# Kernel tuning notes

Hardware: AMD Instinct MI355X
Metric: run time of the kernel (lower is better)

Reference implementation:

```python
import jax, jax.numpy as jnp
import numpy as np

G, NPG = 256, 128          # graphs per batch, nodes per graph
N = G * NPG                # 32768 total nodes
E = 524288                 # total directed edges; first half 'in', second half 'out'
DIN, D = 128, 256          # input feature dim, hidden dim
R = 200                    # num relations
C = 2                      # num classes
EPS = 1e-5                 # batchnorm eps


def setup_inputs() -> dict:
    key = jax.random.key(0)
    ks = jax.random.split(key, 20)

    def w(k, shape):
        fan_in = shape[-2] if len(shape) >= 2 else shape[-1]
        return jax.random.normal(k, shape, jnp.float32) / np.float32(np.sqrt(fan_in))

    return {
        "x": jax.random.normal(ks[0], (N, DIN), jnp.float32),
        "rel_emb": w(ks[1], (R, DIN)),
        # conv1: DIN -> D
        "w_in1": w(ks[2], (DIN, D)), "w_out1": w(ks[3], (DIN, D)),
        "w_loop1": w(ks[4], (DIN, D)), "w_rel1": w(ks[5], (DIN, D)),
        "loop_rel1": w(ks[6], (1, DIN)),
        "bias1": jnp.zeros((D,), jnp.float32),
        "gamma1": jnp.ones((D,), jnp.float32), "beta1": jnp.zeros((D,), jnp.float32),
        # conv2..conv5 stacked: D -> D
        "W_in": w(ks[7], (4, D, D)), "W_out": w(ks[8], (4, D, D)),
        "W_loop": w(ks[9], (4, D, D)), "W_rel": w(ks[10], (4, D, D)),
        "Loop_rel": w(ks[11], (4, 1, D)),
        "Bias": jnp.zeros((4, D), jnp.float32),
        "Gamma": jnp.ones((4, D), jnp.float32), "Beta": jnp.zeros((4, D), jnp.float32),
        # head: concat2 => Linear(4*D, C)
        "lin_w": w(ks[12], (4 * D, C)), "lin_b": jnp.zeros((C,), jnp.float32),
        # graph data (int constants)
        "edge_index": jax.random.randint(ks[13], (2, E), 0, N),
        "edge_type": jax.random.randint(ks[14], (E,), 0, R),
        "batch": jnp.repeat(jnp.arange(G, dtype=jnp.int32), NPG),
        "rel_labels": jax.random.randint(ks[15], (G,), 0, R),
    }


def _compgcn_conv(x, rel, edge_index, edge_type,
                  w_in, w_out, w_loop, w_rel, loop_rel, bias, gamma, beta):
    """One CompGCNConv layer (opn='mult', dropout=identity/eval, BN with batch stats)."""
    n = x.shape[0]
    half = edge_index.shape[1] // 2

    def direction(idx, etype, W):
        src, dst = idx[0], idx[1]
        # symmetric normalization: deg^{-1/2}[src] * deg^{-1/2}[dst]
        deg = jax.ops.segment_sum(jnp.ones_like(src, jnp.float32), src, num_segments=n)
        dinv = jnp.where(deg > 0, deg ** -0.5, 0.0)
        norm = dinv[src] * dinv[dst]                       # [half]
        msg = ((x[src] * rel[etype]) @ W) * norm[:, None]  # [half, D]
        return jax.ops.segment_sum(msg, dst, num_segments=n)

    in_res = direction(edge_index[:, :half], edge_type[:half], w_in)
    out_res = direction(edge_index[:, half:], edge_type[half:], w_out)
    loop_res = (x * loop_rel) @ w_loop                     # self-loop, loop relation, no norm

    out = (in_res + out_res + loop_res) / 3.0 + bias
    mean = out.mean(axis=0)
    var = out.var(axis=0)
    out = (out - mean) / jnp.sqrt(var + EPS) * gamma + beta
    return jax.nn.relu(out), rel @ w_rel


def reference(x, rel_emb, w_in1, w_out1, w_loop1, w_rel1, loop_rel1, bias1, gamma1, beta1,
              W_in, W_out, W_loop, W_rel, Loop_rel, Bias, Gamma, Beta,
              lin_w, lin_b, edge_index, edge_type, batch, rel_labels):
    x, r = _compgcn_conv(x, rel_emb, edge_index, edge_type,
                         w_in1, w_out1, w_loop1, w_rel1, loop_rel1, bias1, gamma1, beta1)
    for l in range(4):  # conv2..conv5 (fixed small layer loop)
        x, r = _compgcn_conv(x, r, edge_index, edge_type,
                             W_in[l], W_out[l], W_loop[l], W_rel[l],
                             Loop_rel[l], Bias[l], Gamma[l], Beta[l])

    # per-graph head/tail nodes (first two nodes of each graph) via segment offsets
    counts = jax.ops.segment_sum(jnp.ones((x.shape[0],), jnp.float32), batch, num_segments=G)
    offsets = (jnp.cumsum(counts) - counts).astype(jnp.int32)
    h_batch = x[offsets]
    t_batch = x[offsets + 1]

    pooled = jax.ops.segment_sum(x, batch, num_segments=G) / counts[:, None]
    rel_embs = r[rel_labels]

    feats = jnp.concatenate([pooled, rel_embs, h_batch, t_batch], axis=1)  # concat2 path
    return feats @ lin_w + lin_b


if __name__ == "__main__":
    out = reference(**setup_inputs())
    print(out.shape, out.dtype)
```

## Files before the change

### kernel.cpp

```cpp
#include <hip/hip_runtime.h>

#define NN 32768
#define GG 256
#define NPGN 128
#define ET 524288
#define EH 262144
#define D1 128
#define D2 256
#define RR 200

typedef unsigned short u16;
typedef __attribute__((ext_vector_type(8))) short bf16x8;
typedef __attribute__((ext_vector_type(4))) float f32x4;
typedef __attribute__((ext_vector_type(8))) unsigned short u16x8;

__device__ __forceinline__ float bf2f(u16 u) {
    union { unsigned int i; float f; } v; v.i = ((unsigned int)u) << 16; return v.f;
}
__device__ __forceinline__ u16 f2bf(float f) {
    union { unsigned int i; float f; } v; v.f = f;
    unsigned int x = v.i;
    return (u16)((x + 0x7fffu + ((x >> 16) & 1u)) >> 16);
}

__global__ void k_hist(const int* __restrict__ ei, int* __restrict__ hs_in,
                       int* __restrict__ hs_out, int* __restrict__ hd_in,
                       int* __restrict__ hd_out) {
    int e = blockIdx.x * blockDim.x + threadIdx.x;
    if (e >= ET) return;
    int s = ei[e], d = ei[ET + e];
    if (e < EH) { atomicAdd(&hs_in[s], 1);  atomicAdd(&hd_in[d], 1); }
    else        { atomicAdd(&hs_out[s], 1); atomicAdd(&hd_out[d], 1); }
}

__global__ void k_dinv(const int* __restrict__ hs_in, const int* __restrict__ hs_out,
                       float* __restrict__ dinv_in, float* __restrict__ dinv_out) {
    int n = blockIdx.x * blockDim.x + threadIdx.x;
    if (n >= NN) return;
    int a = hs_in[n], b = hs_out[n];
    dinv_in[n]  = a > 0 ? rsqrtf((float)a) : 0.f;
    dinv_out[n] = b > 0 ? rsqrtf((float)b) : 0.f;
}

__global__ __launch_bounds__(1024) void k_scan(const int* __restrict__ hist,
                                               int* __restrict__ off) {
    __shared__ int lds[1024];
    int t = threadIdx.x;
    int base = t * 32;
    int loc[32];
    int s = 0;
#pragma unroll
    for (int i = 0; i < 32; ++i) { loc[i] = s; s += hist[base + i]; }
    lds[t] = s;
    int tot = s;
    __syncthreads();
    for (int st = 1; st < 1024; st <<= 1) {
        int v = (t >= st) ? lds[t - st] : 0;
        __syncthreads();
        lds[t] += v;
        __syncthreads();
    }
    int excl = lds[t] - tot;
#pragma unroll
    for (int i = 0; i < 32; ++i) off[base + i] = excl + loc[i];
    if (t == 1023) off[NN] = lds[1023];
}

__global__ void k_fill(const int* __restrict__ ei, const int* __restrict__ et,
                       const float* __restrict__ dinv, const int* __restrict__ off,
                       int* __restrict__ cur, int* __restrict__ c_src,
                       int* __restrict__ c_et, float* __restrict__ c_norm, int eoff) {
    int e = blockIdx.x * blockDim.x + threadIdx.x;
    if (e >= EH) return;
    int s = ei[eoff + e], d = ei[ET + eoff + e], t = et[eoff + e];
    int slot = off[d] + atomicAdd(&cur[d], 1);
    c_src[slot] = s;
    c_et[slot] = t;
    c_norm[slot] = dinv[s] * dinv[d];
}

__global__ void k_convx(const float* __restrict__ in, u16* __restrict__ out, int n) {
    int i = blockIdx.x * blockDim.x + threadIdx.x;
    if (i < n) out[i] = f2bf(in[i]);
}

__global__ __launch_bounds__(256) void k_prepw(
    const float* __restrict__ Wi, const float* __restrict__ Wo,
    const float* __restrict__ Wl, const float* __restrict__ lr,
    u16* __restrict__ WiT, u16* __restrict__ WoT, u16* __restrict__ WlT, int K) {
    __shared__ float tile[32][33];
    const int fam = blockIdx.z;
    const int l = blockIdx.y;
    const int ntiles_n = 256 / 32;
    const int k0 = (blockIdx.x / ntiles_n) * 32;
    const int n0 = (blockIdx.x % ntiles_n) * 32;
    const float* src = fam == 0 ? Wi : fam == 1 ? Wo : Wl;
    u16* dst = fam == 0 ? WiT : fam == 1 ? WoT : WlT;
    const int tn = threadIdx.x & 31, tk = threadIdx.x >> 5;
#pragma unroll
    for (int j = 0; j < 4; ++j) {
        int k = k0 + tk + j * 8;
        tile[tk + j * 8][tn] = src[((size_t)l * K + k) * 256 + n0 + tn];
    }
    __syncthreads();
    const int tk2 = threadIdx.x & 31, tn2 = threadIdx.x >> 5;
    float scale = 1.0f;
    if (fam == 2) scale = lr[(size_t)l * K + k0 + tk2];
#pragma unroll
    for (int j = 0; j < 4; ++j) {
        int n = n0 + tn2 + j * 8;
        dst[((size_t)l * 256 + n) * K + k0 + tk2] = f2bf(tile[tk2][tn2 + j * 8] * scale);
    }
}

template <int K>
__global__ __launch_bounds__(256) void k_gather2(
    const u16* __restrict__ x, const u16* __restrict__ relb,
    const int* __restrict__ csI, const int* __restrict__ cetI,
    const float* __restrict__ cnI, const int* __restrict__ offI,
    const int* __restrict__ csO, const int* __restrict__ cetO,
    const float* __restrict__ cnO, const int* __restrict__ offO,
    u16* __restrict__ aggI, u16* __restrict__ aggO, float* __restrict__ bnsums) {
    if (blockIdx.x == 0 && blockIdx.y == 0 && threadIdx.x < 128)
        ((float4*)bnsums)[threadIdx.x] = make_float4(0.f, 0.f, 0.f, 0.f);
    constexpr int LPN = K / 8;
    constexpr int NPB = 256 / LPN;
    const int dir = blockIdx.y;
    const int* __restrict__ cs  = dir ? csO : csI;
    const int* __restrict__ cet = dir ? cetO : cetI;
    const float* __restrict__ cn = dir ? cnO : cnI;
    const int* __restrict__ off = dir ? offO : offI;
    u16* __restrict__ agg = dir ? aggO : aggI;

    int node = blockIdx.x * NPB + (threadIdx.x / LPN);
    int lane = threadIdx.x % LPN;
    int c = lane * 8;
    int e0 = off[node], e1 = off[node + 1];
    float acc[8] = {};
    int e = e0;
    for (; e + 4 <= e1; e += 4) {
        int s0 = cs[e],  s1 = cs[e + 1],  s2 = cs[e + 2],  s3 = cs[e + 3];
        int t0 = cet[e], t1 = cet[e + 1], t2 = cet[e + 2], t3 = cet[e + 3];
        float n0 = cn[e], n1 = cn[e + 1], n2 = cn[e + 2], n3 = cn[e + 3];
        u16x8 xa = *(const u16x8*)(x + (size_t)s0 * K + c);
        u16x8 xb = *(const u16x8*)(x + (size_t)s1 * K + c);
        u16x8 xc = *(const u16x8*)(x + (size_t)s2 * K + c);
        u16x8 xd = *(const u16x8*)(x + (size_t)s3 * K + c);
        u16x8 ra = *(const u16x8*)(relb + (size_t)t0 * K + c);
        u16x8 rb = *(const u16x8*)(relb + (size_t)t1 * K + c);
        u16x8 rc = *(const u16x8*)(relb + (size_t)t2 * K + c);
        u16x8 rd = *(const u16x8*)(relb + (size_t)t3 * K + c);
#pragma unroll
        for (int i = 0; i < 8; ++i)
            acc[i] += n0 * bf2f(xa[i]) * bf2f(ra[i]) + n1 * bf2f(xb[i]) * bf2f(rb[i])
                    + n2 * bf2f(xc[i]) * bf2f(rc[i]) + n3 * bf2f(xd[i]) * bf2f(rd[i]);
    }
    for (; e < e1; ++e) {
        int s0 = cs[e], t0 = cet[e]; float n0 = cn[e];
        u16x8 xa = *(const u16x8*)(x + (size_t)s0 * K + c);
        u16x8 ra = *(const u16x8*)(relb + (size_t)t0 * K + c);
#pragma unroll
        for (int i = 0; i < 8; ++i) acc[i] += n0 * bf2f(xa[i]) * bf2f(ra[i]);
    }
    u16x8 o;
#pragma unroll
    for (int i = 0; i < 8; ++i) o[i] = f2bf(acc[i]);
    *(u16x8*)(agg + (size_t)node * K + c) = o;
}

__device__ __forceinline__ void stage16(const u16* __restrict__ src, int baseRow,
                                        int K, int kk, u16* lds, int chunk, int lane) {
    int row = chunk * 16 + (lane >> 2);
    int ks  = (lane & 3) ^ ((lane >> 2) & 3);
    const u16* g = src + (size_t)(baseRow + row) * K + kk + ks * 8;
    __builtin_amdgcn_global_load_lds((const __attribute__((address_space(1))) void*)g,
                                     (__attribute__((address_space(3))) void*)(lds + chunk * 512),
                                     16, 0, 0);
}

template <int K>
__global__ __launch_bounds__(256) void k_gemm_mfma(
    const u16* __restrict__ A1, const u16* __restrict__ A2, const u16* __restrict__ A3,
    const u16* __restrict__ W1, const u16* __restrict__ W2, const u16* __restrict__ W3,
    const float* __restrict__ bias, u16* __restrict__ hb, float* __restrict__ bnsums) {
    __shared__ u16 As_s[2][128 * 32];
    __shared__ u16 Ws_s[2][64 * 32];
    const int tid = threadIdx.x;
    const int wave = tid >> 6, lane = tid & 63;
    const int q = lane >> 4, r = lane & 15;
    const int rowBlk = blockIdx.x * 128;
    const int colBlk = blockIdx.y * 64;
    const int rowBase = rowBlk + (wave & 1) * 64;
    const int colSub  = (wave >> 1) * 32;

    f32x4 zero = {0.f, 0.f, 0.f, 0.f};
    f32x4 acc[4][2];
#pragma unroll
    for (int i = 0; i < 4; ++i)
#pragma unroll
        for (int j = 0; j < 2; ++j) acc[i][j] = zero;

    const u16* As[3] = {A1, A2, A3};
    const u16* Ws[3] = {W1, W2, W3};
    constexpr int SPS = K / 32;
    constexpr int TOT = 3 * SPS;

    stage16(As[0], rowBlk, K, 0, As_s[0], 2 * wave, lane);
    stage16(As[0], rowBlk, K, 0, As_s[0], 2 * wave + 1, lane);
    stage16(Ws[0], colBlk, K, 0, Ws_s[0], wave, lane);

    const int sw = (q ^ (r & 3)) * 8;
    for (int s = 0; s < TOT; ++s) {
        __syncthreads();
        if (s + 1 < TOT) {
            int seg = (s + 1) / SPS;
            int kk  = ((s + 1) % SPS) * 32;
            stage16(As[seg], rowBlk, K, kk, As_s[(s + 1) & 1], 2 * wave, lane);
            stage16(As[seg], rowBlk, K, kk, As_s[(s + 1) & 1], 2 * wave + 1, lane);
            stage16(Ws[seg], colBlk, K, kk, Ws_s[(s + 1) & 1], wave, lane);
        }
        const u16* al = As_s[s & 1] + (wave & 1) * 64 * 32;
        const u16* wl = Ws_s[s & 1] + colSub * 32;
        bf16x8 a[4], b[2];
#pragma unroll
        for (int t = 0; t < 4; ++t) a[t] = *(const bf16x8*)(al + (t * 16 + r) * 32 + sw);
#pragma unroll
        for (int t = 0; t < 2; ++t) b[t] = *(const bf16x8*)(wl + (t * 16 + r) * 32 + sw);
#pragma unroll
        for (int tm = 0; tm < 4; ++tm)
#pragma unroll
            for (int tn = 0; tn < 2; ++tn)
                acc[tm][tn] = __builtin_amdgcn_mfma_f32_16x16x32_bf16(
                    a[tm], b[tn], acc[tm][tn], 0, 0, 0);
    }

#pragma unroll
    for (int tn = 0; tn < 2; ++tn) {
        int col = colBlk + colSub + tn * 16 + r;
        float bv = bias[col];
        float sv = 0.f, qv = 0.f;
#pragma unroll
        for (int tm = 0; tm < 4; ++tm) {
#pragma unroll
            for (int reg = 0; reg < 4; ++reg) {
                int row = rowBase + tm * 16 + q * 4 + reg;
                float v = acc[tm][tn][reg] * (1.0f / 3.0f) + bv;
                hb[(size_t)row * 256 + col] = f2bf(v);
                sv += v; qv += v * v;
            }
        }
        sv += __shfl_xor(sv, 16); sv += __shfl_xor(sv, 32);
        qv += __shfl_xor(qv, 16); qv += __shfl_xor(qv, 32);
        if (q == 0) {
            atomicAdd(&bnsums[col], sv);
            atomicAdd(&bnsums[256 + col], qv);
        }
    }
}

__global__ __launch_bounds__(256) void k_gemm_rel(
    const float* __restrict__ A, const float* __restrict__ W,
    float* __restrict__ C, u16* __restrict__ Cb, int M, int K) {
    __shared__ float As[16][68];
    __shared__ float Wshm[16][68];
    const int tid = threadIdx.x;
    const int tx = tid & 15, ty = tid >> 4;
    const int arow = tid >> 2;
    const int akc  = (tid & 3) << 2;
    const int wk   = tid >> 4;
    const int wn0  = (tid & 15) << 2;
    const int rowBase = blockIdx.x << 6;
    const int colBase = blockIdx.y << 6;
    float acc[4][4] = {};
    for (int k0 = 0; k0 < K; k0 += 16) {
        float4 av = make_float4(0.f, 0.f, 0.f, 0.f);
        int rr = rowBase + arow;
        if (rr < M) av = *(const float4*)(A + (size_t)rr * K + k0 + akc);
        As[akc + 0][arow] = av.x;
        As[akc + 1][arow] = av.y;
        As[akc + 2][arow] = av.z;
        As[akc + 3][arow] = av.w;
        float4 wv = *(const float4*)(W + (size_t)(k0 + wk) * D2 + colBase + wn0);
        Wshm[wk][wn0 + 0] = wv.x;
        Wshm[wk][wn0 + 1] = wv.y;
        Wshm[wk][wn0 + 2] = wv.z;
        Wshm[wk][wn0 + 3] = wv.w;
        __syncthreads();
#pragma unroll
        for (int kk = 0; kk < 16; ++kk) {
            float a0 = As[kk][(ty << 2) + 0], a1 = As[kk][(ty << 2) + 1];
            float a2 = As[kk][(ty << 2) + 2], a3 = As[kk][(ty << 2) + 3];
            float w0 = Wshm[kk][(tx << 2) + 0], w1 = Wshm[kk][(tx << 2) + 1];
            float w2 = Wshm[kk][(tx << 2) + 2], w3 = Wshm[kk][(tx << 2) + 3];
            acc[0][0] += a0 * w0; acc[0][1] += a0 * w1; acc[0][2] += a0 * w2; acc[0][3] += a0 * w3;
            acc[1][0] += a1 * w0; acc[1][1] += a1 * w1; acc[1][2] += a1 * w2; acc[1][3] += a1 * w3;
            acc[2][0] += a2 * w0; acc[2][1] += a2 * w1; acc[2][2] += a2 * w2; acc[2][3] += a2 * w3;
            acc[3][0] += a3 * w0; acc[3][1] += a3 * w1; acc[3][2] += a3 * w2; acc[3][3] += a3 * w3;
        }
        __syncthreads();
    }
#pragma unroll
    for (int i = 0; i < 4; ++i) {
        int rr = rowBase + (ty << 2) + i;
        if (rr >= M) continue;
        float* cp = C + (size_t)rr * D2 + colBase + (tx << 2);
        u16* cb = Cb + (size_t)rr * D2 + colBase + (tx << 2);
        cp[0] = acc[i][0]; cp[1] = acc[i][1]; cp[2] = acc[i][2]; cp[3] = acc[i][3];
        cb[0] = f2bf(acc[i][0]); cb[1] = f2bf(acc[i][1]);
        cb[2] = f2bf(acc[i][2]); cb[3] = f2bf(acc[i][3]);
    }
}

__global__ void k_bnapply(const u16x8* __restrict__ hb8, const float* __restrict__ sums,
                          const float* __restrict__ gamma, const float* __restrict__ beta,
                          u16x8* __restrict__ xb8) {
    int idx = blockIdx.x * blockDim.x + threadIdx.x;
    int f0 = (idx & 31) << 3;
    u16x8 v = hb8[idx];
    u16x8 o;
#pragma unroll
    for (int i = 0; i < 8; ++i) {
        int f = f0 + i;
        float mean = sums[f] * (1.0f / NN);
        float var  = sums[256 + f] * (1.0f / NN) - mean * mean;
        float inv  = 1.0f / sqrtf(var + 1e-5f);
        float t = (bf2f(v[i]) - mean) * inv * gamma[f] + beta[f];
        o[i] = f2bf(t > 0.f ? t : 0.f);
    }
    xb8[idx] = o;
}

__global__ void k_feats(const u16* __restrict__ x, const float* __restrict__ rel,
                        const int* __restrict__ rel_labels, float* __restrict__ feats) {
    int g = blockIdx.x, f = threadIdx.x;
    const u16* xg = x + (size_t)g * NPGN * D2;
    float s = 0.f;
#pragma unroll 8
    for (int n = 0; n < NPGN; ++n) s += bf2f(xg[(size_t)n * D2 + f]);
    float* fg = feats + (size_t)g * 1024;
    fg[f]       = s * (1.0f / NPGN);
    fg[256 + f] = rel[(size_t)rel_labels[g] * D2 + f];
    fg[512 + f] = bf2f(xg[f]);
    fg[768 + f] = bf2f(xg[D2 + f]);
}

__global__ void k_head(const float* __restrict__ feats, const float* __restrict__ lw,
                       const float* __restrict__ lb, float* __restrict__ out) {
    int g = blockIdx.x, t = threadIdx.x;
    __shared__ float s0[256], s1[256];
    float a0 = 0.f, a1 = 0.f;
#pragma unroll
    for (int j = 0; j < 4; ++j) {
        int k = t * 4 + j;
        float fv = feats[(size_t)g * 1024 + k];
        a0 += fv * lw[k * 2 + 0];
        a1 += fv * lw[k * 2 + 1];
    }
    s0[t] = a0; s1[t] = a1;
    __syncthreads();
    for (int s = 128; s > 0; s >>= 1) {
        if (t < s) { s0[t] += s0[t + s]; s1[t] += s1[t + s]; }
        __syncthreads();
    }
    if (t == 0) {
        out[g * 2 + 0] = s0[0] + lb[0];
        out[g * 2 + 1] = s1[0] + lb[1];
    }
}

extern "C" void kernel_launch(void* const* d_in, const int* in_sizes, int n_in,
                              void* d_out, int out_size, void* d_ws, size_t ws_size,
                              hipStream_t stream) {
    const float* x0   = (const float*)d_in[0];
    const float* rel0 = (const float*)d_in[1];
    const int* edge_index = (const int*)d_in[20];
    const int* edge_type  = (const int*)d_in[21];
    const int* rel_labels = (const int*)d_in[23];
    float* out = (float*)d_out;

    float* ws = (float*)d_ws;
    float* relA  = ws;
    float* relB  = relA + (size_t)RR * 256;
    float* dinv_in  = relB + (size_t)RR * 256;
    float* dinv_out = dinv_in + NN;
    float* cnorm_in  = dinv_out + NN;
    float* cnorm_out = cnorm_in + EH;
    float* bnsums    = cnorm_out + EH;
    float* feats     = bnsums + 512;
    int* csrc_in  = (int*)(feats + GG * 1024);
    int* cet_in   = csrc_in + EH;
    int* csrc_out = cet_in + EH;
    int* cet_out  = csrc_out + EH;
    int* off_in   = cet_out + EH;
    int* off_out  = off_in + NN + 8;
    int* hs_in    = off_out + NN + 8;
    int* hs_out   = hs_in + NN;
    int* hd_in    = hs_out + NN;
    int* hd_out   = hd_in + NN;
    int* cur_in   = hd_out + NN;
    int* cur_out  = cur_in + NN;
    u16* xbf0 = (u16*)(cur_out + NN);
    u16* xbfA = xbf0 + (size_t)NN * 128;
    u16* aggI = xbfA + (size_t)NN * 256;
    u16* aggO = aggI + (size_t)NN * 256;
    u16* hb   = aggO + (size_t)NN * 256;
    u16* wt0  = hb + (size_t)NN * 256;
    u16* wtS  = wt0 + 3 * 256 * 128;
    u16* relbf = wtS + 12 * 65536;

    hipMemsetAsync(hs_in, 0, 6 * NN * sizeof(int), stream);
    k_hist<<<ET / 256, 256, 0, stream>>>(edge_index, hs_in, hs_out, hd_in, hd_out);
    k_dinv<<<NN / 256, 256, 0, stream>>>(hs_in, hs_out, dinv_in, dinv_out);
    k_scan<<<1, 1024, 0, stream>>>(hd_in, off_in);
    k_scan<<<1, 1024, 0, stream>>>(hd_out, off_out);
    k_fill<<<EH / 256, 256, 0, stream>>>(edge_index, edge_type, dinv_in, off_in,
                                         cur_in, csrc_in, cet_in, cnorm_in, 0);
    k_fill<<<EH / 256, 256, 0, stream>>>(edge_index, edge_type, dinv_out, off_out,
                                         cur_out, csrc_out, cet_out, cnorm_out, EH);
    k_convx<<<(NN * D1) / 256, 256, 0, stream>>>(x0, xbf0, NN * D1);
    k_convx<<<(RR * D1 + 255) / 256, 256, 0, stream>>>(rel0, relbf, RR * D1);
    {
        dim3 g0((D1 / 32) * 8, 1, 3);
        k_prepw<<<g0, 256, 0, stream>>>(
            (const float*)d_in[2], (const float*)d_in[3], (const float*)d_in[4],
            (const float*)d_in[6], wt0, wt0 + 256 * D1, wt0 + 2 * 256 * D1, D1);
        dim3 gS((D2 / 32) * 8, 4, 3);
        k_prepw<<<gS, 256, 0, stream>>>(
            (const float*)d_in[10], (const float*)d_in[11], (const float*)d_in[12],
            (const float*)d_in[14], wtS, wtS + 4 * 65536, wtS + 8 * 65536, D2);
    }

    const float* rc = rel0; float* rn = relA;

    for (int l = 0; l < 5; ++l) {
        const int K = (l == 0) ? D1 : D2;
        const u16* xb = (l == 0) ? xbf0 : xbfA;
        const u16 *WiT, *WoT, *WlT;
        const float *Wr, *bias, *gamma, *beta;
        if (l == 0) {
            WiT = wt0; WoT = wt0 + 256 * D1; WlT = wt0 + 2 * 256 * D1;
            Wr = (const float*)d_in[5];
            bias  = (const float*)d_in[7];
            gamma = (const float*)d_in[8];
            beta  = (const float*)d_in[9];
        } else {
            int m = l - 1;
            WiT = wtS + (size_t)m * 65536;
            WoT = wtS + (size_t)(4 + m) * 65536;
            WlT = wtS + (size_t)(8 + m) * 65536;
            Wr = (const float*)d_in[13] + (size_t)m * D2 * D2;
            bias  = (const float*)d_in[15] + (size_t)m * D2;
            gamma = (const float*)d_in[16] + (size_t)m * D2;
            beta  = (const float*)d_in[17] + (size_t)m * D2;
        }

        if (K == D1) {
            dim3 ggr(NN / 16, 2);
            k_gather2<D1><<<ggr, 256, 0, stream>>>(xb, relbf, csrc_in, cet_in,
                cnorm_in, off_in, csrc_out, cet_out, cnorm_out, off_out, aggI, aggO, bnsums);
        } else {
            dim3 ggr(NN / 8, 2);
            k_gather2<D2><<<ggr, 256, 0, stream>>>(xb, relbf, csrc_in, cet_in,
                cnorm_in, off_in, csrc_out, cet_out, cnorm_out, off_out, aggI, aggO, bnsums);
        }
        dim3 ggrid(NN / 128, 4);
        if (K == D1) k_gemm_mfma<D1><<<ggrid, 256, 0, stream>>>(aggI, aggO, xb, WiT, WoT, WlT, bias, hb, bnsums);
        else         k_gemm_mfma<D2><<<ggrid, 256, 0, stream>>>(aggI, aggO, xb, WiT, WoT, WlT, bias, hb, bnsums);
        k_bnapply<<<(NN * 256 / 8) / 256, 256, 0, stream>>>((const u16x8*)hb, bnsums,
                                                            gamma, beta, (u16x8*)xbfA);
        k_gemm_rel<<<dim3(4, 4), 256, 0, stream>>>(rc, Wr, rn, relbf, RR, K);
        const float* nr = rn;
        rn = (l == 0) ? relB : (float*)rc;
        rc = nr;
    }

    k_feats<<<GG, 256, 0, stream>>>(xbfA, rc, rel_labels, feats);
    k_head<<<GG, 256, 0, stream>>>(feats, (const float*)d_in[18],
                                   (const float*)d_in[19], out);
}
```

Before: 814.4 us.

## Enlarge GEMM tile to 128x128 and merge small setup and BN/rel launches

The main MFMA GEMM moves from a 128x64 block tile to a 128x128 tile, so each wave computes a 64x64 subtile with 16 accumulators. This halves the grid and reduces how often the A operands are re-read from global memory. Separately, the paired scan, fill and convert launches are merged into single launches, and the BN-apply kernel is fused with the relation GEMM into one launch to cut launch overhead. The larger tile raises register use and halves the number of blocks, which could lower occupancy and leave the GPU underfilled.

```diff
diff --git a/kernel.cpp b/kernel.cpp
--- a/kernel.cpp
+++ b/kernel.cpp
@@ -42,8 +42,12 @@
     dinv_out[n] = b > 0 ? rsqrtf((float)b) : 0.f;
 }
 
-__global__ __launch_bounds__(1024) void k_scan(const int* __restrict__ hist,
-                                               int* __restrict__ off) {
+__global__ __launch_bounds__(1024) void k_scan2(const int* __restrict__ hdI,
+                                                const int* __restrict__ hdO,
+                                                int* __restrict__ offI,
+                                                int* __restrict__ offO) {
+    const int* __restrict__ hist = blockIdx.x ? hdO : hdI;
+    int* __restrict__ off = blockIdx.x ? offO : offI;
     __shared__ int lds[1024];
     int t = threadIdx.x;
     int base = t * 32;
@@ -66,12 +70,23 @@
     if (t == 1023) off[NN] = lds[1023];
 }
 
-__global__ void k_fill(const int* __restrict__ ei, const int* __restrict__ et,
-                       const float* __restrict__ dinv, const int* __restrict__ off,
-                       int* __restrict__ cur, int* __restrict__ c_src,
-                       int* __restrict__ c_et, float* __restrict__ c_norm, int eoff) {
+__global__ void k_fill2(const int* __restrict__ ei, const int* __restrict__ et,
+                        const float* __restrict__ dinvI, const float* __restrict__ dinvO,
+                        const int* __restrict__ offI, const int* __restrict__ offO,
+                        int* __restrict__ curI, int* __restrict__ curO,
+                        int* __restrict__ csI, int* __restrict__ csO,
+                        int* __restrict__ cetI, int* __restrict__ cetO,
+                        float* __restrict__ cnI, float* __restrict__ cnO) {
     int e = blockIdx.x * blockDim.x + threadIdx.x;
     if (e >= EH) return;
+    const int dir = blockIdx.y;
+    const float* __restrict__ dinv = dir ? dinvO : dinvI;
+    const int* __restrict__ off = dir ? offO : offI;
+    int* __restrict__ cur = dir ? curO : curI;
+    int* __restrict__ c_src = dir ? csO : csI;
+    int* __restrict__ c_et = dir ? cetO : cetI;
+    float* __restrict__ c_norm = dir ? cnO : cnI;
+    const int eoff = dir ? EH : 0;
     int s = ei[eoff + e], d = ei[ET + eoff + e], t = et[eoff + e];
     int slot = off[d] + atomicAdd(&cur[d], 1);
     c_src[slot] = s;
@@ -79,9 +94,11 @@
     c_norm[slot] = dinv[s] * dinv[d];
 }
 
-__global__ void k_convx(const float* __restrict__ in, u16* __restrict__ out, int n) {
+__global__ void k_conv2(const float* __restrict__ a, u16* __restrict__ oa, int na,
+                        const float* __restrict__ b, u16* __restrict__ ob, int nb) {
     int i = blockIdx.x * blockDim.x + threadIdx.x;
-    if (i < n) out[i] = f2bf(in[i]);
+    if (i < na) oa[i] = f2bf(a[i]);
+    else if (i < na + nb) ob[i - na] = f2bf(b[i - na]);
 }
 
 __global__ __launch_bounds__(256) void k_prepw(
@@ -184,21 +201,21 @@
     const u16* __restrict__ W1, const u16* __restrict__ W2, const u16* __restrict__ W3,
     const float* __restrict__ bias, u16* __restrict__ hb, float* __restrict__ bnsums) {
     __shared__ u16 As_s[2][128 * 32];
-    __shared__ u16 Ws_s[2][64 * 32];
+    __shared__ u16 Ws_s[2][128 * 32];
     const int tid = threadIdx.x;
     const int wave = tid >> 6, lane = tid & 63;
     const int q = lane >> 4, r = lane & 15;
     const int rowBlk = blockIdx.x * 128;
-    const int colBlk = blockIdx.y * 64;
+    const int colBlk = blockIdx.y * 128;
     const int rowBase = rowBlk + (wave & 1) * 64;
-    const int colSub  = (wave >> 1) * 32;
+    const int colBase = colBlk + (wave >> 1) * 64;
 
     f32x4 zero = {0.f, 0.f, 0.f, 0.f};
-    f32x4 acc[4][2];
+    f32x4 acc[4][4];
 #pragma unroll
     for (int i = 0; i < 4; ++i)
 #pragma unroll
-        for (int j = 0; j < 2; ++j) acc[i][j] = zero;
+        for (int j = 0; j < 4; ++j) acc[i][j] = zero;
 
     const u16* As[3] = {A1, A2, A3};
     const u16* Ws[3] = {W1, W2, W3};
@@ -207,7 +224,8 @@
 
     stage16(As[0], rowBlk, K, 0, As_s[0], 2 * wave, lane);
     stage16(As[0], rowBlk, K, 0, As_s[0], 2 * wave + 1, lane);
-    stage16(Ws[0], colBlk, K, 0, Ws_s[0], wave, lane);
+    stage16(Ws[0], colBlk, K, 0, Ws_s[0], 2 * wave, lane);
+    stage16(Ws[0], colBlk, K, 0, Ws_s[0], 2 * wave + 1, lane);
 
     const int sw = (q ^ (r & 3)) * 8;
     for (int s = 0; s < TOT; ++s) {
@@ -217,26 +235,28 @@
             int kk  = ((s + 1) % SPS) * 32;
             stage16(As[seg], rowBlk, K, kk, As_s[(s + 1) & 1], 2 * wave, lane);
             stage16(As[seg], rowBlk, K, kk, As_s[(s + 1) & 1], 2 * wave + 1, lane);
-            stage16(Ws[seg], colBlk, K, kk, Ws_s[(s + 1) & 1], wave, lane);
+            stage16(Ws[seg], colBlk, K, kk, Ws_s[(s + 1) & 1], 2 * wave, lane);
+            stage16(Ws[seg], colBlk, K, kk, Ws_s[(s + 1) & 1], 2 * wave + 1, lane);
         }
         const u16* al = As_s[s & 1] + (wave & 1) * 64 * 32;
-        const u16* wl = Ws_s[s & 1] + colSub * 32;
-        bf16x8 a[4], b[2];
-#pragma unroll
-        for (int t = 0; t < 4; ++t) a[t] = *(const bf16x8*)(al + (t * 16 + r) * 32 + sw);
-#pragma unroll
-        for (int t = 0; t < 2; ++t) b[t] = *(const bf16x8*)(wl + (t * 16 + r) * 32 + sw);
+        const u16* wl = Ws_s[s & 1] + (wave >> 1) * 64 * 32;
+        bf16x8 a[4], b[4];
+#pragma unroll
+        for (int t = 0; t < 4; ++t) {
+            a[t] = *(const bf16x8*)(al + (t * 16 + r) * 32 + sw);
+            b[t] = *(const bf16x8*)(wl + (t * 16 + r) * 32 + sw);
+        }
 #pragma unroll
         for (int tm = 0; tm < 4; ++tm)
 #pragma unroll
-            for (int tn = 0; tn < 2; ++tn)
+            for (int tn = 0; tn < 4; ++tn)
                 acc[tm][tn] = __builtin_amdgcn_mfma_f32_16x16x32_bf16(
                     a[tm], b[tn], acc[tm][tn], 0, 0, 0);
     }
 
 #pragma unroll
-    for (int tn = 0; tn < 2; ++tn) {
-        int col = colBlk + colSub + tn * 16 + r;
+    for (int tn = 0; tn < 4; ++tn) {
+        int col = colBase + tn * 16 + r;
         float bv = bias[col];
         float sv = 0.f, qv = 0.f;
 #pragma unroll
@@ -258,19 +278,40 @@
     }
 }
 
-__global__ __launch_bounds__(256) void k_gemm_rel(
+__global__ __launch_bounds__(256) void k_bnrel(
+    const u16x8* __restrict__ hb8, const float* __restrict__ sums,
+    const float* __restrict__ gamma, const float* __restrict__ beta,
+    u16x8* __restrict__ xb8,
     const float* __restrict__ A, const float* __restrict__ W,
     float* __restrict__ C, u16* __restrict__ Cb, int M, int K) {
     __shared__ float As[16][68];
     __shared__ float Wshm[16][68];
+    if (blockIdx.x < 4096) {
+        int idx = blockIdx.x * 256 + threadIdx.x;
+        int f0 = (idx & 31) << 3;
+        u16x8 v = hb8[idx];
+        u16x8 o;
+#pragma unroll
+        for (int i = 0; i < 8; ++i) {
+            int f = f0 + i;
+            float mean = sums[f] * (1.0f / NN);
+            float var  = sums[256 + f] * (1.0f / NN) - mean * mean;
+            float inv  = 1.0f / sqrtf(var + 1e-5f);
+            float t = (bf2f(v[i]) - mean) * inv * gamma[f] + beta[f];
+            o[i] = f2bf(t > 0.f ? t : 0.f);
+        }
+        xb8[idx] = o;
+        return;
+    }
+    const int bx = blockIdx.x - 4096;
+    const int rowBase = (bx & 3) << 6;
+    const int colBase = (bx >> 2) << 6;
     const int tid = threadIdx.x;
     const int tx = tid & 15, ty = tid >> 4;
     const int arow = tid >> 2;
     const int akc  = (tid & 3) << 2;
     const int wk   = tid >> 4;
     const int wn0  = (tid & 15) << 2;
-    const int rowBase = blockIdx.x << 6;
-    const int colBase = blockIdx.y << 6;
     float acc[4][4] = {};
     for (int k0 = 0; k0 < K; k0 += 16) {
         float4 av = make_float4(0.f, 0.f, 0.f, 0.f);
@@ -309,25 +350,6 @@
         cb[0] = f2bf(acc[i][0]); cb[1] = f2bf(acc[i][1]);
         cb[2] = f2bf(acc[i][2]); cb[3] = f2bf(acc[i][3]);
     }
-}
-
-__global__ void k_bnapply(const u16x8* __restrict__ hb8, const float* __restrict__ sums,
-                          const float* __restrict__ gamma, const float* __restrict__ beta,
-                          u16x8* __restrict__ xb8) {
-    int idx = blockIdx.x * blockDim.x + threadIdx.x;
-    int f0 = (idx & 31) << 3;
-    u16x8 v = hb8[idx];
-    u16x8 o;
-#pragma unroll
-    for (int i = 0; i < 8; ++i) {
-        int f = f0 + i;
-        float mean = sums[f] * (1.0f / NN);
-        float var  = sums[256 + f] * (1.0f / NN) - mean * mean;
-        float inv  = 1.0f / sqrtf(var + 1e-5f);
-        float t = (bf2f(v[i]) - mean) * inv * gamma[f] + beta[f];
-        o[i] = f2bf(t > 0.f ? t : 0.f);
-    }
-    xb8[idx] = o;
 }
 
 __global__ void k_feats(const u16* __restrict__ x, const float* __restrict__ rel,
@@ -411,14 +433,12 @@
     hipMemsetAsync(hs_in, 0, 6 * NN * sizeof(int), stream);
     k_hist<<<ET / 256, 256, 0, stream>>>(edge_index, hs_in, hs_out, hd_in, hd_out);
     k_dinv<<<NN / 256, 256, 0, stream>>>(hs_in, hs_out, dinv_in, dinv_out);
-    k_scan<<<1, 1024, 0, stream>>>(hd_in, off_in);
-    k_scan<<<1, 1024, 0, stream>>>(hd_out, off_out);
-    k_fill<<<EH / 256, 256, 0, stream>>>(edge_index, edge_type, dinv_in, off_in,
-                                         cur_in, csrc_in, cet_in, cnorm_in, 0);
-    k_fill<<<EH / 256, 256, 0, stream>>>(edge_index, edge_type, dinv_out, off_out,
-                                         cur_out, csrc_out, cet_out, cnorm_out, EH);
-    k_convx<<<(NN * D1) / 256, 256, 0, stream>>>(x0, xbf0, NN * D1);
-    k_convx<<<(RR * D1 + 255) / 256, 256, 0, stream>>>(rel0, relbf, RR * D1);
+    k_scan2<<<2, 1024, 0, stream>>>(hd_in, hd_out, off_in, off_out);
+    k_fill2<<<dim3(EH / 256, 2), 256, 0, stream>>>(edge_index, edge_type,
+        dinv_in, dinv_out, off_in, off_out, cur_in, cur_out,
+        csrc_in, csrc_out, cet_in, cet_out, cnorm_in, cnorm_out);
+    k_conv2<<<(NN * D1 + RR * D1 + 255) / 256, 256, 0, stream>>>(
+        x0, xbf0, NN * D1, rel0, relbf, RR * D1);
     {
         dim3 g0((D1 / 32) * 8, 1, 3);
         k_prepw<<<g0, 256, 0, stream>>>(
@@ -463,12 +483,11 @@
             k_gather2<D2><<<ggr, 256, 0, stream>>>(xb, relbf, csrc_in, cet_in,
                 cnorm_in, off_in, csrc_out, cet_out, cnorm_out, off_out, aggI, aggO, bnsums);
         }
-        dim3 ggrid(NN / 128, 4);
+        dim3 ggrid(NN / 128, 2);
         if (K == D1) k_gemm_mfma<D1><<<ggrid, 256, 0, stream>>>(aggI, aggO, xb, WiT, WoT, WlT, bias, hb, bnsums);
         else         k_gemm_mfma<D2><<<ggrid, 256, 0, stream>>>(aggI, aggO, xb, WiT, WoT, WlT, bias, hb, bnsums);
-        k_bnapply<<<(NN * 256 / 8) / 256, 256, 0, stream>>>((const u16x8*)hb, bnsums,
-                                                            gamma, beta, (u16x8*)xbfA);
-        k_gemm_rel<<<dim3(4, 4), 256, 0, stream>>>(rc, Wr, rn, relbf, RR, K);
+        k_bnrel<<<4096 + 16, 256, 0, stream>>>((const u16x8*)hb, bnsums, gamma, beta,
+                                               (u16x8*)xbfA, rc, Wr, rn, relbf, RR, K);
         const float* nr = rn;
         rn = (l == 0) ? relB : (float*)rc;
         rc = nr;
```

Result: faster. 773.6 us (-5.0%).
